# Kernel tuning notes

Hardware: AMD Instinct MI355X
Metric: run time of the kernel (lower is better)

The kernel has to match this reference:

```python
import jax, jax.numpy as jnp
import numpy as np

B, C, H, W_IMG = 64, 3, 512, 512
P = 16                      # patch size
IN_F, OUT_F, HEADS = 256, 64, 8
HD = HEADS * OUT_F          # 512
PATCH_DIM = P * P * C       # 768
EPS = 1e-5


def setup_inputs() -> dict:
    key = jax.random.key(0)
    ks = jax.random.split(key, 11)
    s = 0.02
    return {
        "token": jax.random.normal(ks[0], (B, IN_F), jnp.float32),
        "feature": jax.random.normal(ks[1], (B, C, H, W_IMG), jnp.float32),
        "W_patch": jax.random.normal(ks[2], (PATCH_DIM, IN_F), jnp.float32) * s,
        "b_patch": jax.random.normal(ks[3], (IN_F,), jnp.float32) * s,
        "W": jax.random.normal(ks[4], (IN_F, HD), jnp.float32) * s,
        "a_self": jax.random.normal(ks[5], (HEADS, OUT_F), jnp.float32) * s,
        "a_neigh": jax.random.normal(ks[6], (HEADS, OUT_F), jnp.float32) * s,
        "W_out": jax.random.normal(ks[7], (HD, IN_F), jnp.float32) * s,
        "b_out": jax.random.normal(ks[8], (IN_F,), jnp.float32) * s,
        "gamma": jnp.ones((IN_F,), jnp.float32),
        "beta": jnp.zeros((IN_F,), jnp.float32),
    }


def _forward(token, feature, W_patch, b_patch, W, a_self, a_neigh, W_out, b_out, gamma, beta):
    b = token.shape[0]
    # to_patch: 'b c (h p1) (w p2) -> b (h w) (p1 p2 c)' then Linear
    hh, ww = H // P, W_IMG // P
    patches = feature.reshape(b, C, hh, P, ww, P)
    patches = patches.transpose(0, 2, 4, 3, 5, 1).reshape(b, hh * ww, P * P * C)
    feat = patches @ W_patch + b_patch                    # [b, n, IN_F]
    feat_h = (feat @ W).reshape(b, -1, HEADS, OUT_F).transpose(0, 2, 1, 3)  # [b, h, n, d]
    tok_h = (token @ W).reshape(b, HEADS, OUT_F)          # [b, h, d]
    # per-head GAT-style scores (vectorized over heads)
    a_s = jnp.einsum('bhd,hd->bh', tok_h, a_self)         # [b, h]
    a_n = jnp.einsum('bhnd,hd->bhn', feat_h, a_neigh)     # [b, h, n]
    attn = jax.nn.leaky_relu(a_s[:, :, None] + a_n, 0.2)  # [b, h, n]
    # original: softmax over the trailing size-1 axis -> all ones (faithful)
    attn = jax.nn.softmax(attn[..., None], axis=-1)[..., 0]
    out = jnp.einsum('bhn,bhnd->bhd', attn, feat_h)       # [b, h, d]
    # concat=True branch
    out = 0.5 * (out.reshape(b, HD) @ W_out + b_out) + 0.5 * token
    x = 0.5 * out + 0.5 * token
    mu = jnp.mean(x, axis=-1, keepdims=True)
    var = jnp.mean((x - mu) ** 2, axis=-1, keepdims=True)
    return (x - mu) * jax.lax.rsqrt(var + EPS) * gamma + beta


def reference(token, feature, W_patch, b_patch, W, a_self, a_neigh, W_out, b_out, gamma, beta):
    return _forward(token, feature, W_patch, b_patch, W, a_self, a_neigh, W_out, b_out, gamma, beta)
```

## Files before the change

### kernel.cpp

```cpp
#include <hip/hip_runtime.h>

#define BB 64
#define CC 3
#define HH 512
#define WW 512
#define PP 16
#define IN_F 256
#define HD 512
#define PATCH_DIM 768
#define NPATCH 1024
#define NB_M2 512

typedef float floatx4 __attribute__((ext_vector_type(4)));


__global__ __launch_bounds__(256)
void prep_kernel(const float* __restrict__ feature,
                 const float* __restrict__ W,
                 const float* __restrict__ Wo,
                 float* __restrict__ S,
                 float* __restrict__ M2)
{
    int bid = blockIdx.x;
    int t = threadIdx.x;

    if (bid < NB_M2) {
        __shared__ float sW[HD];
        __shared__ float part[4][128];

        int i  = bid >> 1;
        int ct = bid & 1;

        sW[t]       = W[(size_t)i * HD + t];
        sW[t + 256] = W[(size_t)i * HD + t + 256];
        __syncthreads();

        int tc = t & 63;
        int kg = t >> 6;
        int j  = ct * 128 + tc * 2;

        float a0 = 0.f, a1 = 0.f;
        const float* wb = Wo + j;
#pragma unroll 8
        for (int k = kg * 128; k < kg * 128 + 128; ++k) {
            float2 w = *(const float2*)(wb + (size_t)k * IN_F);
            float s = sW[k];
            a0 += s * w.x;
            a1 += s * w.y;
        }
        part[kg][tc * 2]     = a0;
        part[kg][tc * 2 + 1] = a1;
        __syncthreads();

        if (t < 128) {
            float s = part[0][t] + part[1][t] + part[2][t] + part[3][t];
            M2[(size_t)i * IN_F + ct * 128 + t] = s;
        }
        return;
    }

    {
        int pbid = bid - NB_M2;
        int p1 = pbid & 15;
        int tmp = pbid >> 4;
        int c = tmp % 3;
        int b = tmp / 3;

        const size_t base_bc = (size_t)(b * 3 + c) * (size_t)(HH * WW);

        float acc[4] = {0.f, 0.f, 0.f, 0.f};

#pragma unroll
        for (int i = 0; i < 16; ++i) {
            int idx = i * 256 + t;
            int h = idx >> 7;
            int u = idx & 127;
            size_t off = base_bc + (size_t)(p1 + 16 * h) * WW + (size_t)u * 4;
            floatx4 v = __builtin_nontemporal_load((const floatx4*)(feature + off));
            acc[0] += v.x;
            acc[1] += v.y;
            acc[2] += v.z;
            acc[3] += v.w;
        }

        __shared__ float red[16 * 68];
        __shared__ float red2[16 * 8];
        int g = t >> 2;
        int pb = (t & 3) * 4;
#pragma unroll
        for (int j = 0; j < 4; ++j)
            red[(pb + j) * 68 + g] = acc[j];
        __syncthreads();

        if (t < 128) {
            int bin = t >> 3;
            int l = t & 7;
            float s = 0.f;
#pragma unroll
            for (int q = 0; q < 8; ++q)
                s += red[bin * 68 + l + 8 * q];
            red2[bin * 8 + l] = s;
        }
        __syncthreads();

        if (t < 16) {
            float s = 0.f;
#pragma unroll
            for (int l = 0; l < 8; ++l)
                s += red2[t * 8 + l];
            S[(size_t)b * PATCH_DIM + (size_t)(p1 * 16 + t) * 3 + c] = s;
        }
    }
}

__global__ __launch_bounds__(512)
void fuse_kernel(const float* __restrict__ S,
                 const float* __restrict__ Wp,
                 const float* __restrict__ bp,
                 const float* __restrict__ M2,
                 const float* __restrict__ bo,
                 const float* __restrict__ tok,
                 const float* __restrict__ gamma,
                 const float* __restrict__ beta,
                 float* __restrict__ out)
{
    int b = blockIdx.x;
    int t = threadIdx.x;

    __shared__ float sS[PATCH_DIM];
    __shared__ float part1[8 * IN_F];
    __shared__ float sT[IN_F];
    __shared__ float part2[8 * IN_F];
    __shared__ float wred[8];
    __shared__ float stats[2];

    float bo_t = 0.f, tok_t = 0.f, gamma_t = 0.f, beta_t = 0.f, bp_t = 0.f;
    if (t < IN_F) {
        bo_t    = bo[t];
        tok_t   = tok[b * IN_F + t];
        gamma_t = gamma[t];
        beta_t  = beta[t];
        bp_t    = bp[t];
    }

    for (int k = t; k < PATCH_DIM; k += 512)
        sS[k] = S[(size_t)b * PATCH_DIM + k];
    __syncthreads();

    {
        int j4 = (t & 63) * 4;
        int kg = t >> 6;
        float a0 = 0.f, a1 = 0.f, a2 = 0.f, a3 = 0.f;
        const float* wrow = Wp + (size_t)(kg * 96) * IN_F + j4;
#pragma unroll 8
        for (int i = 0; i < 96; ++i) {
            float s = sS[kg * 96 + i];
            float4 w = *(const float4*)(wrow + (size_t)i * IN_F);
            a0 += s * w.x; a1 += s * w.y; a2 += s * w.z; a3 += s * w.w;
        }
        part1[kg * IN_F + j4 + 0] = a0;
        part1[kg * IN_F + j4 + 1] = a1;
        part1[kg * IN_F + j4 + 2] = a2;
        part1[kg * IN_F + j4 + 3] = a3;
    }
    __syncthreads();
    if (t < IN_F) {
        float s = 0.f;
#pragma unroll
        for (int kg = 0; kg < 8; ++kg)
            s += part1[kg * IN_F + t];
        sT[t] = s + 1024.f * bp_t;
    }
    __syncthreads();

    {
        int j4 = (t & 63) * 4;
        int kg = t >> 6;
        float a0 = 0.f, a1 = 0.f, a2 = 0.f, a3 = 0.f;
        const float* wrow = M2 + (size_t)(kg * 32) * IN_F + j4;
#pragma unroll 8
        for (int i = 0; i < 32; ++i) {
            float s = sT[kg * 32 + i];
            float4 w = *(const float4*)(wrow + (size_t)i * IN_F);
            a0 += s * w.x; a1 += s * w.y; a2 += s * w.z; a3 += s * w.w;
        }
        part2[kg * IN_F + j4 + 0] = a0;
        part2[kg * IN_F + j4 + 1] = a1;
        part2[kg * IN_F + j4 + 2] = a2;
        part2[kg * IN_F + j4 + 3] = a3;
    }
    __syncthreads();

    float x = 0.f;
    if (t < IN_F) {
        float z = 0.f;
#pragma unroll
        for (int kg = 0; kg < 8; ++kg)
            z += part2[kg * IN_F + t];
        x = 0.25f * (z + bo_t) + 0.75f * tok_t;
    }

    float s1 = x, s2 = x * x;
#pragma unroll
    for (int off = 32; off > 0; off >>= 1) {
        s1 += __shfl_down(s1, off);
        s2 += __shfl_down(s2, off);
    }
    int wave = t >> 6;
    if ((t & 63) == 0 && wave < 4) {
        wred[wave * 2]     = s1;
        wred[wave * 2 + 1] = s2;
    }
    __syncthreads();
    if (t == 0) {
        float a1 = wred[0] + wred[2] + wred[4] + wred[6];
        float a2 = wred[1] + wred[3] + wred[5] + wred[7];
        float mu = a1 * (1.f / 256.f);
        float var = a2 * (1.f / 256.f) - mu * mu;
        stats[0] = mu;
        stats[1] = rsqrtf(var + 1e-5f);
    }
    __syncthreads();

    if (t < IN_F) {
        float y = (x - stats[0]) * stats[1] * gamma_t + beta_t;
        out[b * IN_F + t] = y;
    }
}

extern "C" void kernel_launch(void* const* d_in, const int* in_sizes, int n_in,
                              void* d_out, int out_size, void* d_ws, size_t ws_size,
                              hipStream_t stream)
{
    const float* token   = (const float*)d_in[0];
    const float* feature = (const float*)d_in[1];
    const float* W_patch = (const float*)d_in[2];
    const float* b_patch = (const float*)d_in[3];
    const float* W       = (const float*)d_in[4];
    const float* W_out   = (const float*)d_in[7];
    const float* b_out   = (const float*)d_in[8];
    const float* gamma   = (const float*)d_in[9];
    const float* beta    = (const float*)d_in[10];

    float* out = (float*)d_out;
    float* S  = (float*)d_ws;
    float* M2 = S + (size_t)BB * PATCH_DIM;

    dim3 grid1(NB_M2 + BB * CC * 16);
    prep_kernel<<<grid1, 256, 0, stream>>>(feature, W, W_out, S, M2);

    fuse_kernel<<<BB, 512, 0, stream>>>(S, W_patch, b_patch, M2, b_out,
                                        token, gamma, beta, out);
}
```

Baseline: 295.8 us.

## Merge prep and fuse kernels into one launch with atomic-counter dependencies

Folds the per-batch fuse stage into the prep kernel as extra trailing blocks that spin on agent-scope atomic counters until their batch's 48 patch-sum blocks and all 512 M2 blocks have signalled. The aim is to drop the second kernel launch and its inter-kernel gap, so fuse work for early batches can overlap the remaining streaming. A memset of the counters is added, and fuse blocks now use 256 threads with twice the loop length per thread. The design assumes blocks are scheduled in index order, otherwise a spinning fuse block could occupy a slot needed by a producer.

```diff
diff --git a/kernel.cpp b/kernel.cpp
--- a/kernel.cpp
+++ b/kernel.cpp
@@ -8,25 +8,34 @@
 #define IN_F 256
 #define HD 512
 #define PATCH_DIM 768
-#define NPATCH 1024
 #define NB_M2 512
+#define NB_PATCH (BB * CC * 16)
+#define NB_FUSE BB
 
 typedef float floatx4 __attribute__((ext_vector_type(4)));
 
 
 __global__ __launch_bounds__(256)
-void prep_kernel(const float* __restrict__ feature,
+void mega_kernel(const float* __restrict__ feature,
                  const float* __restrict__ W,
                  const float* __restrict__ Wo,
+                 const float* __restrict__ Wp,
+                 const float* __restrict__ bp,
+                 const float* __restrict__ bo,
+                 const float* __restrict__ tok,
+                 const float* __restrict__ gamma,
+                 const float* __restrict__ beta,
                  float* __restrict__ S,
-                 float* __restrict__ M2)
+                 float* __restrict__ M2,
+                 int* __restrict__ ctr,
+                 float* __restrict__ out)
 {
     int bid = blockIdx.x;
     int t = threadIdx.x;
 
     if (bid < NB_M2) {
         __shared__ float sW[HD];
-        __shared__ float part[4][128];
+        __shared__ float partm[4][128];
 
         int i  = bid >> 1;
         int ct = bid & 1;
@@ -48,18 +57,22 @@
             a0 += s * w.x;
             a1 += s * w.y;
         }
-        part[kg][tc * 2]     = a0;
-        part[kg][tc * 2 + 1] = a1;
+        partm[kg][tc * 2]     = a0;
+        partm[kg][tc * 2 + 1] = a1;
         __syncthreads();
 
         if (t < 128) {
-            float s = part[0][t] + part[1][t] + part[2][t] + part[3][t];
+            float s = partm[0][t] + partm[1][t] + partm[2][t] + partm[3][t];
             M2[(size_t)i * IN_F + ct * 128 + t] = s;
         }
+        __syncthreads();
+        if (t == 0)
+            __hip_atomic_fetch_add(&ctr[BB], 1, __ATOMIC_RELEASE,
+                                   __HIP_MEMORY_SCOPE_AGENT);
         return;
     }
 
-    {
+    if (bid < NB_M2 + NB_PATCH) {
         int pbid = bid - NB_M2;
         int p1 = pbid & 15;
         int tmp = pbid >> 4;
@@ -110,119 +123,108 @@
                 s += red2[t * 8 + l];
             S[(size_t)b * PATCH_DIM + (size_t)(p1 * 16 + t) * 3 + c] = s;
         }
+        __syncthreads();
+        if (t == 0)
+            __hip_atomic_fetch_add(&ctr[b], 1, __ATOMIC_RELEASE,
+                                   __HIP_MEMORY_SCOPE_AGENT);
+        return;
     }
-}
-
-__global__ __launch_bounds__(512)
-void fuse_kernel(const float* __restrict__ S,
-                 const float* __restrict__ Wp,
-                 const float* __restrict__ bp,
-                 const float* __restrict__ M2,
-                 const float* __restrict__ bo,
-                 const float* __restrict__ tok,
-                 const float* __restrict__ gamma,
-                 const float* __restrict__ beta,
-                 float* __restrict__ out)
-{
-    int b = blockIdx.x;
-    int t = threadIdx.x;
-
-    __shared__ float sS[PATCH_DIM];
-    __shared__ float part1[8 * IN_F];
-    __shared__ float sT[IN_F];
-    __shared__ float part2[8 * IN_F];
-    __shared__ float wred[8];
-    __shared__ float stats[2];
-
-    float bo_t = 0.f, tok_t = 0.f, gamma_t = 0.f, beta_t = 0.f, bp_t = 0.f;
-    if (t < IN_F) {
-        bo_t    = bo[t];
-        tok_t   = tok[b * IN_F + t];
-        gamma_t = gamma[t];
-        beta_t  = beta[t];
-        bp_t    = bp[t];
-    }
-
-    for (int k = t; k < PATCH_DIM; k += 512)
-        sS[k] = S[(size_t)b * PATCH_DIM + k];
-    __syncthreads();
 
     {
-        int j4 = (t & 63) * 4;
-        int kg = t >> 6;
-        float a0 = 0.f, a1 = 0.f, a2 = 0.f, a3 = 0.f;
-        const float* wrow = Wp + (size_t)(kg * 96) * IN_F + j4;
+        int b = bid - (NB_M2 + NB_PATCH);
+
+        __shared__ float sS[PATCH_DIM];
+        __shared__ float part1[4 * IN_F];
+        __shared__ float sT[IN_F];
+        __shared__ float part2[4 * IN_F];
+        __shared__ float wred[8];
+        __shared__ float stats[2];
+
+        float bo_t    = bo[t];
+        float tok_t   = tok[b * IN_F + t];
+        float gamma_t = gamma[t];
+        float beta_t  = beta[t];
+        float bp_t    = bp[t];
+
+        if (t == 0) {
+            while (__hip_atomic_load(&ctr[b], __ATOMIC_ACQUIRE,
+                                     __HIP_MEMORY_SCOPE_AGENT) < 48 ||
+                   __hip_atomic_load(&ctr[BB], __ATOMIC_ACQUIRE,
+                                     __HIP_MEMORY_SCOPE_AGENT) < NB_M2) {
+                __builtin_amdgcn_s_sleep(8);
+            }
+        }
+        __syncthreads();
+
+        for (int k = t; k < PATCH_DIM; k += 256)
+            sS[k] = S[(size_t)b * PATCH_DIM + k];
+        __syncthreads();
+
+        {
+            int j4 = (t & 63) * 4;
+            int kg = t >> 6;
+            float a0 = 0.f, a1 = 0.f, a2 = 0.f, a3 = 0.f;
+            const float* wrow = Wp + (size_t)(kg * 192) * IN_F + j4;
 #pragma unroll 8
-        for (int i = 0; i < 96; ++i) {
-            float s = sS[kg * 96 + i];
-            float4 w = *(const float4*)(wrow + (size_t)i * IN_F);
-            a0 += s * w.x; a1 += s * w.y; a2 += s * w.z; a3 += s * w.w;
-        }
-        part1[kg * IN_F + j4 + 0] = a0;
-        part1[kg * IN_F + j4 + 1] = a1;
-        part1[kg * IN_F + j4 + 2] = a2;
-        part1[kg * IN_F + j4 + 3] = a3;
-    }
-    __syncthreads();
-    if (t < IN_F) {
-        float s = 0.f;
-#pragma unroll
-        for (int kg = 0; kg < 8; ++kg)
-            s += part1[kg * IN_F + t];
-        sT[t] = s + 1024.f * bp_t;
-    }
-    __syncthreads();
-
-    {
-        int j4 = (t & 63) * 4;
-        int kg = t >> 6;
-        float a0 = 0.f, a1 = 0.f, a2 = 0.f, a3 = 0.f;
-        const float* wrow = M2 + (size_t)(kg * 32) * IN_F + j4;
+            for (int i = 0; i < 192; ++i) {
+                float s = sS[kg * 192 + i];
+                float4 w = *(const float4*)(wrow + (size_t)i * IN_F);
+                a0 += s * w.x; a1 += s * w.y; a2 += s * w.z; a3 += s * w.w;
+            }
+            part1[kg * IN_F + j4 + 0] = a0;
+            part1[kg * IN_F + j4 + 1] = a1;
+            part1[kg * IN_F + j4 + 2] = a2;
+            part1[kg * IN_F + j4 + 3] = a3;
+        }
+        __syncthreads();
+        sT[t] = part1[t] + part1[IN_F + t] + part1[2 * IN_F + t]
+              + part1[3 * IN_F + t] + 1024.f * bp_t;
+        __syncthreads();
+
+        {
+            int j4 = (t & 63) * 4;
+            int kg = t >> 6;
+            float a0 = 0.f, a1 = 0.f, a2 = 0.f, a3 = 0.f;
+            const float* wrow = M2 + (size_t)(kg * 64) * IN_F + j4;
 #pragma unroll 8
-        for (int i = 0; i < 32; ++i) {
-            float s = sT[kg * 32 + i];
-            float4 w = *(const float4*)(wrow + (size_t)i * IN_F);
-            a0 += s * w.x; a1 += s * w.y; a2 += s * w.z; a3 += s * w.w;
-        }
-        part2[kg * IN_F + j4 + 0] = a0;
-        part2[kg * IN_F + j4 + 1] = a1;
-        part2[kg * IN_F + j4 + 2] = a2;
-        part2[kg * IN_F + j4 + 3] = a3;
-    }
-    __syncthreads();
-
-    float x = 0.f;
-    if (t < IN_F) {
-        float z = 0.f;
-#pragma unroll
-        for (int kg = 0; kg < 8; ++kg)
-            z += part2[kg * IN_F + t];
-        x = 0.25f * (z + bo_t) + 0.75f * tok_t;
-    }
-
-    float s1 = x, s2 = x * x;
-#pragma unroll
-    for (int off = 32; off > 0; off >>= 1) {
-        s1 += __shfl_down(s1, off);
-        s2 += __shfl_down(s2, off);
-    }
-    int wave = t >> 6;
-    if ((t & 63) == 0 && wave < 4) {
-        wred[wave * 2]     = s1;
-        wred[wave * 2 + 1] = s2;
-    }
-    __syncthreads();
-    if (t == 0) {
-        float a1 = wred[0] + wred[2] + wred[4] + wred[6];
-        float a2 = wred[1] + wred[3] + wred[5] + wred[7];
-        float mu = a1 * (1.f / 256.f);
-        float var = a2 * (1.f / 256.f) - mu * mu;
-        stats[0] = mu;
-        stats[1] = rsqrtf(var + 1e-5f);
-    }
-    __syncthreads();
-
-    if (t < IN_F) {
+            for (int i = 0; i < 64; ++i) {
+                float s = sT[kg * 64 + i];
+                float4 w = *(const float4*)(wrow + (size_t)i * IN_F);
+                a0 += s * w.x; a1 += s * w.y; a2 += s * w.z; a3 += s * w.w;
+            }
+            part2[kg * IN_F + j4 + 0] = a0;
+            part2[kg * IN_F + j4 + 1] = a1;
+            part2[kg * IN_F + j4 + 2] = a2;
+            part2[kg * IN_F + j4 + 3] = a3;
+        }
+        __syncthreads();
+
+        float z = part2[t] + part2[IN_F + t] + part2[2 * IN_F + t]
+                + part2[3 * IN_F + t];
+        float x = 0.25f * (z + bo_t) + 0.75f * tok_t;
+
+        float s1 = x, s2 = x * x;
+#pragma unroll
+        for (int off = 32; off > 0; off >>= 1) {
+            s1 += __shfl_down(s1, off);
+            s2 += __shfl_down(s2, off);
+        }
+        int wave = t >> 6;
+        if ((t & 63) == 0) {
+            wred[wave * 2]     = s1;
+            wred[wave * 2 + 1] = s2;
+        }
+        __syncthreads();
+        if (t == 0) {
+            float a1 = wred[0] + wred[2] + wred[4] + wred[6];
+            float a2 = wred[1] + wred[3] + wred[5] + wred[7];
+            float mu = a1 * (1.f / 256.f);
+            float var = a2 * (1.f / 256.f) - mu * mu;
+            stats[0] = mu;
+            stats[1] = rsqrtf(var + 1e-5f);
+        }
+        __syncthreads();
+
         float y = (x - stats[0]) * stats[1] * gamma_t + beta_t;
         out[b * IN_F + t] = y;
     }
@@ -243,12 +245,14 @@
     const float* beta    = (const float*)d_in[10];
 
     float* out = (float*)d_out;
-    float* S  = (float*)d_ws;
-    float* M2 = S + (size_t)BB * PATCH_DIM;
-
-    dim3 grid1(NB_M2 + BB * CC * 16);
-    prep_kernel<<<grid1, 256, 0, stream>>>(feature, W, W_out, S, M2);
-
-    fuse_kernel<<<BB, 512, 0, stream>>>(S, W_patch, b_patch, M2, b_out,
-                                        token, gamma, beta, out);
+    float* S   = (float*)d_ws;
+    float* M2  = S + (size_t)BB * PATCH_DIM;
+    int*   ctr = (int*)(M2 + (size_t)IN_F * IN_F);
+
+    hipMemsetAsync(ctr, 0, (BB + 1) * sizeof(int), stream);
+
+    dim3 grid(NB_M2 + NB_PATCH + NB_FUSE);
+    mega_kernel<<<grid, 256, 0, stream>>>(feature, W, W_out, W_patch, b_patch,
+                                          b_out, token, gamma, beta,
+                                          S, M2, ctr, out);
 }
```

After: 453.5 us. 53.3% more time.
